# Kernel tuning notes

Measured on AMD Instinct MI355X. Metric: run time of the kernel, lower is better.

Reference implementation:

```python
import jax, jax.numpy as jnp
import numpy as np

V, C, H, W = 6, 256, 128, 128


def setup_inputs() -> dict:
    key = jax.random.key(0)
    ks = jax.random.split(key, 6)
    return {
        "q": jax.random.normal(ks[0], (V, C, H, W), dtype=jnp.float32),
        "k": jax.random.normal(ks[1], (V, C, H, W), dtype=jnp.float32),
        "v": jax.random.normal(ks[2], (V, C, H, W), dtype=jnp.float32),
        "Wq": jax.random.normal(ks[3], (C, C), dtype=jnp.float32) * (1.0 / np.sqrt(C)),
        "Wk": jax.random.normal(ks[4], (C, C), dtype=jnp.float32) * (1.0 / np.sqrt(C)),
        "Wv": jax.random.normal(ks[5], (C, C), dtype=jnp.float32) * (1.0 / np.sqrt(C)),
    }


def reference(q, k, v, Wq, Wk, Wv):
    # 1x1 conv (no bias) == channel GEMM: [V,C,H,W] x [O,C] -> [V,O,H,W]
    qp = jnp.einsum("vchw,oc->vohw", q, Wq)
    kp = jnp.einsum("vchw,oc->vohw", k, Wk)
    vp = jnp.einsum("vchw,oc->vohw", v, Wv)
    # elementwise q*k, sum over channels (dim=1, keepdim) -> [V,1,H,W]
    att = jnp.sum(qp * kp, axis=1, keepdims=True)
    # softmax over views (dim=0)
    att = jax.nn.softmax(att, axis=0)
    # weight values and sum over views (dim=0, keepdim) -> [1,C,H,W]
    out = jnp.sum(att * vp, axis=0, keepdims=True)
    return out
```

## Files before the change

### kernel.cpp

```cpp
#include <hip/hip_runtime.h>
#include <math.h>

#define HW 16384
#define C_DIM 256
#define V_DIM 6
#define PT 64
#define BK 32
#define KROW 40

typedef short bf16x8 __attribute__((ext_vector_type(8)));
typedef float f32x4 __attribute__((ext_vector_type(4)));

__device__ __forceinline__ void split2(float x, unsigned short& h,
                                       unsigned short& l) {
    unsigned u = __float_as_uint(x);
    h = (unsigned short)(u >> 16);
    float xl = x - __uint_as_float(u & 0xFFFF0000u);
    l = (unsigned short)(__float_as_uint(xl) >> 16);
}

__global__ void compute_M_kernel(const float* __restrict__ Wq,
                                 const float* __restrict__ Wk,
                                 unsigned short* __restrict__ Mh,
                                 unsigned short* __restrict__ Ml) {
    const int i = blockIdx.x;
    const int j = threadIdx.x;
    float a0 = 0.f, a1 = 0.f, a2 = 0.f, a3 = 0.f;
    #pragma unroll 4
    for (int o = 0; o < C_DIM; o += 4) {
        a0 = fmaf(Wq[(o + 0) * C_DIM + i], Wk[(o + 0) * C_DIM + j], a0);
        a1 = fmaf(Wq[(o + 1) * C_DIM + i], Wk[(o + 1) * C_DIM + j], a1);
        a2 = fmaf(Wq[(o + 2) * C_DIM + i], Wk[(o + 2) * C_DIM + j], a2);
        a3 = fmaf(Wq[(o + 3) * C_DIM + i], Wk[(o + 3) * C_DIM + j], a3);
    }
    float acc = (a0 + a1) + (a2 + a3);
    unsigned short h, l;
    split2(acc, h, l);
    Mh[i * C_DIM + j] = h;
    Ml[i * C_DIM + j] = l;
}

__global__ __launch_bounds__(512, 4) void score_kernel(
        const float* __restrict__ q, const float* __restrict__ k,
        const unsigned short* __restrict__ Mh,
        const unsigned short* __restrict__ Ml,
        float* __restrict__ score) {
    const int tid  = threadIdx.x;
    const int lane = tid & 63;
    const int w    = tid >> 6;
    const int pt   = blockIdx.x & 255;
    const int v    = blockIdx.x >> 8;
    const int gp0  = pt * PT;
    const int l15  = lane & 15;
    const int l4   = lane >> 4;

    __shared__ __align__(16) unsigned short Kh_s[2][PT * KROW];
    __shared__ __align__(16) unsigned short Kl_s[2][PT * KROW];
    __shared__ float s_red[8][PT];

    const float* kv = k + (size_t)v * C_DIM * HW + gp0;
    const float* qv = q + (size_t)v * C_DIM * HW + gp0;
    const int ibase = w * 32;

    f32x4 acc[2][4];
    #pragma unroll
    for (int a = 0; a < 2; ++a)
        #pragma unroll
        for (int b = 0; b < 4; ++b)
            acc[a][b] = (f32x4){0.f, 0.f, 0.f, 0.f};

    float kx[2][4];
    bf16x8 Ah[2][2], Al[2][2];

    {
        const float* kp = kv + (size_t)(w * 4) * HW + lane;
        float x[4];
        #pragma unroll
        for (int e = 0; e < 4; ++e) x[e] = kp[(size_t)e * HW];
        unsigned short h[4], l[4];
        #pragma unroll
        for (int e = 0; e < 4; ++e) split2(x[e], h[e], l[e]);
        uint2 H, L;
        H.x = (unsigned)h[0] | ((unsigned)h[1] << 16);
        H.y = (unsigned)h[2] | ((unsigned)h[3] << 16);
        L.x = (unsigned)l[0] | ((unsigned)l[1] << 16);
        L.y = (unsigned)l[2] | ((unsigned)l[3] << 16);
        *(uint2*)&Kh_s[0][lane * KROW + w * 4] = H;
        *(uint2*)&Kl_s[0][lane * KROW + w * 4] = L;

        const float* kp1 = kv + (size_t)(BK + w * 4) * HW + lane;
        #pragma unroll
        for (int e = 0; e < 4; ++e) kx[1][e] = kp1[(size_t)e * HW];

        #pragma unroll
        for (int it = 0; it < 2; ++it) {
            int row = ibase + it * 16 + l15;
            Ah[0][it] = *(const bf16x8*)(Mh + (size_t)row * C_DIM + l4 * 8);
            Al[0][it] = *(const bf16x8*)(Ml + (size_t)row * C_DIM + l4 * 8);
        }
    }
    __syncthreads();

    #pragma unroll
    for (int ks = 0; ks < 8; ++ks) {
        const int cur = ks & 1;

        if (ks < 7) {
            #pragma unroll
            for (int it = 0; it < 2; ++it) {
                int row = ibase + it * 16 + l15;
                Ah[cur ^ 1][it] = *(const bf16x8*)(Mh + (size_t)row * C_DIM +
                                                   (ks + 1) * BK + l4 * 8);
                Al[cur ^ 1][it] = *(const bf16x8*)(Ml + (size_t)row * C_DIM +
                                                   (ks + 1) * BK + l4 * 8);
            }
        }
        if (ks < 6) {
            const float* kp = kv + (size_t)((ks + 2) * BK + w * 4) * HW + lane;
            #pragma unroll
            for (int e = 0; e < 4; ++e) kx[cur][e] = kp[(size_t)e * HW];
        }

        bf16x8 Bh[4];
        #pragma unroll
        for (int jt = 0; jt < 4; ++jt) {
            int bp = jt * 16 + l15;
            Bh[jt] = *(const bf16x8*)&Kh_s[cur][bp * KROW + l4 * 8];
        }
        #pragma unroll
        for (int it = 0; it < 2; ++it)
            #pragma unroll
            for (int jt = 0; jt < 4; ++jt)
                acc[it][jt] = __builtin_amdgcn_mfma_f32_16x16x32_bf16(
                                  Ah[cur][it], Bh[jt], acc[it][jt], 0, 0, 0);
        #pragma unroll
        for (int it = 0; it < 2; ++it)
            #pragma unroll
            for (int jt = 0; jt < 4; ++jt)
                acc[it][jt] = __builtin_amdgcn_mfma_f32_16x16x32_bf16(
                                  Al[cur][it], Bh[jt], acc[it][jt], 0, 0, 0);
        bf16x8 Bl[4];
        #pragma unroll
        for (int jt = 0; jt < 4; ++jt) {
            int bp = jt * 16 + l15;
            Bl[jt] = *(const bf16x8*)&Kl_s[cur][bp * KROW + l4 * 8];
        }
        #pragma unroll
        for (int it = 0; it < 2; ++it)
            #pragma unroll
            for (int jt = 0; jt < 4; ++jt)
                acc[it][jt] = __builtin_amdgcn_mfma_f32_16x16x32_bf16(
                                  Ah[cur][it], Bl[jt], acc[it][jt], 0, 0, 0);

        if (ks < 7) {
            unsigned short h[4], l[4];
            #pragma unroll
            for (int e = 0; e < 4; ++e) split2(kx[cur ^ 1][e], h[e], l[e]);
            uint2 H, L;
            H.x = (unsigned)h[0] | ((unsigned)h[1] << 16);
            H.y = (unsigned)h[2] | ((unsigned)h[3] << 16);
            L.x = (unsigned)l[0] | ((unsigned)l[1] << 16);
            L.y = (unsigned)l[2] | ((unsigned)l[3] << 16);
            *(uint2*)&Kh_s[cur ^ 1][lane * KROW + w * 4] = H;
            *(uint2*)&Kl_s[cur ^ 1][lane * KROW + w * 4] = L;
        }
        __syncthreads();
    }

    float sp[4];
    #pragma unroll
    for (int jt = 0; jt < 4; ++jt) sp[jt] = 0.f;
    #pragma unroll
    for (int jt = 0; jt < 4; ++jt) {
        #pragma unroll
        for (int it = 0; it < 2; ++it) {
            int irow = ibase + it * 16 + l4 * 4;
            const float* qp = qv + (size_t)irow * HW + jt * 16 + l15;
            #pragma unroll
            for (int r = 0; r < 4; ++r)
                sp[jt] = fmaf(qp[(size_t)r * HW], acc[it][jt][r], sp[jt]);
        }
        sp[jt] += __shfl_xor(sp[jt], 16, 64);
        sp[jt] += __shfl_xor(sp[jt], 32, 64);
    }
    if (lane < 16) {
        #pragma unroll
        for (int jt = 0; jt < 4; ++jt)
            s_red[w][jt * 16 + lane] = sp[jt];
    }
    __syncthreads();
    if (tid < PT) {
        float s = 0.f;
        #pragma unroll
        for (int ww = 0; ww < 8; ++ww) s += s_red[ww][tid];
        score[v * HW + gp0 + tid] = s;
    }
}

__global__ __launch_bounds__(256) void softmax_w_kernel(float* __restrict__ score) {
    const int p = blockIdx.x * 256 + threadIdx.x;
    float s[V_DIM];
    float mx = -1e30f;
    #pragma unroll
    for (int vv = 0; vv < V_DIM; ++vv) {
        s[vv] = score[vv * HW + p];
        mx = fmaxf(mx, s[vv]);
    }
    float sum = 0.f;
    #pragma unroll
    for (int vv = 0; vv < V_DIM; ++vv) {
        s[vv] = __expf(s[vv] - mx);
        sum += s[vv];
    }
    float inv = 1.0f / sum;
    #pragma unroll
    for (int vv = 0; vv < V_DIM; ++vv)
        score[vv * HW + p] = s[vv] * inv;
}

__global__ void wsplit_kernel(const float* __restrict__ Wv,
                              unsigned short* __restrict__ Wvh,
                              unsigned short* __restrict__ Wvl) {
    const int i = blockIdx.x;
    const int j = threadIdx.x;
    unsigned short h, l;
    split2(Wv[i * C_DIM + j], h, l);
    Wvh[i * C_DIM + j] = h;
    Wvl[i * C_DIM + j] = l;
}

__global__ __launch_bounds__(512, 2) void out_gemm_kernel(
        const float* __restrict__ vin,
        const unsigned short* __restrict__ Wvh,
        const unsigned short* __restrict__ Wvl,
        const float* __restrict__ wsm,
        float* __restrict__ out) {
    const int tid  = threadIdx.x;
    const int lane = tid & 63;
    const int w    = tid >> 6;
    const int gp0  = blockIdx.x * PT;
    const int l15  = lane & 15;
    const int l4   = lane >> 4;
    const int p_s  = tid & 63;
    const int jg   = tid >> 6;

    __shared__ __align__(16) unsigned short Xh_s[2][PT * KROW];
    __shared__ __align__(16) unsigned short Xl_s[2][PT * KROW];

    float wr[V_DIM];
    #pragma unroll
    for (int vv = 0; vv < V_DIM; ++vv) wr[vv] = wsm[vv * HW + gp0 + p_s];

    const float* vbase = vin + gp0 + p_s;
    const int obase = w * 32;

    f32x4 acc[2][4];
    #pragma unroll
    for (int a = 0; a < 2; ++a)
        #pragma unroll
        for (int b = 0; b < 4; ++b)
            acc[a][b] = (f32x4){0.f, 0.f, 0.f, 0.f};

    bf16x8 Ah[2][2], Al[2][2];

    {
        float xv[4][V_DIM];
        #pragma unroll
        for (int vv = 0; vv < V_DIM; ++vv)
            #pragma unroll
            for (int e = 0; e < 4; ++e)
                xv[e][vv] = vbase[(size_t)(vv * C_DIM + jg * 4 + e) * HW];
        unsigned short h[4], l[4];
        #pragma unroll
        for (int e = 0; e < 4; ++e) {
            float s = 0.f;
            #pragma unroll
            for (int vv = 0; vv < V_DIM; ++vv) s = fmaf(wr[vv], xv[e][vv], s);
            split2(s, h[e], l[e]);
        }
        uint2 H, L;
        H.x = (unsigned)h[0] | ((unsigned)h[1] << 16);
        H.y = (unsigned)h[2] | ((unsigned)h[3] << 16);
        L.x = (unsigned)l[0] | ((unsigned)l[1] << 16);
        L.y = (unsigned)l[2] | ((unsigned)l[3] << 16);
        *(uint2*)&Xh_s[0][p_s * KROW + jg * 4] = H;
        *(uint2*)&Xl_s[0][p_s * KROW + jg * 4] = L;

        #pragma unroll
        for (int it = 0; it < 2; ++it) {
            int row = obase + it * 16 + l15;
            Ah[0][it] = *(const bf16x8*)(Wvh + (size_t)row * C_DIM + l4 * 8);
            Al[0][it] = *(const bf16x8*)(Wvl + (size_t)row * C_DIM + l4 * 8);
        }
    }
    __syncthreads();

    #pragma unroll
    for (int ks = 0; ks < 8; ++ks) {
        const int cur = ks & 1;

        float xv[4][V_DIM];
        if (ks < 7) {
            #pragma unroll
            for (int vv = 0; vv < V_DIM; ++vv)
                #pragma unroll
                for (int e = 0; e < 4; ++e)
                    xv[e][vv] = vbase[(size_t)(vv * C_DIM + (ks + 1) * BK +
                                               jg * 4 + e) * HW];
            #pragma unroll
            for (int it = 0; it < 2; ++it) {
                int row = obase + it * 16 + l15;
                Ah[cur ^ 1][it] = *(const bf16x8*)(Wvh + (size_t)row * C_DIM +
                                                   (ks + 1) * BK + l4 * 8);
                Al[cur ^ 1][it] = *(const bf16x8*)(Wvl + (size_t)row * C_DIM +
                                                   (ks + 1) * BK + l4 * 8);
            }
        }

        bf16x8 Bh[4], Bl[4];
        #pragma unroll
        for (int jt = 0; jt < 4; ++jt) {
            int bp = jt * 16 + l15;
            Bh[jt] = *(const bf16x8*)&Xh_s[cur][bp * KROW + l4 * 8];
            Bl[jt] = *(const bf16x8*)&Xl_s[cur][bp * KROW + l4 * 8];
        }

        #pragma unroll
        for (int it = 0; it < 2; ++it)
            #pragma unroll
            for (int jt = 0; jt < 4; ++jt)
                acc[it][jt] = __builtin_amdgcn_mfma_f32_16x16x32_bf16(
                                  Ah[cur][it], Bh[jt], acc[it][jt], 0, 0, 0);
        #pragma unroll
        for (int it = 0; it < 2; ++it)
            #pragma unroll
            for (int jt = 0; jt < 4; ++jt)
                acc[it][jt] = __builtin_amdgcn_mfma_f32_16x16x32_bf16(
                                  Ah[cur][it], Bl[jt], acc[it][jt], 0, 0, 0);
        #pragma unroll
        for (int it = 0; it < 2; ++it)
            #pragma unroll
            for (int jt = 0; jt < 4; ++jt)
                acc[it][jt] = __builtin_amdgcn_mfma_f32_16x16x32_bf16(
                                  Al[cur][it], Bh[jt], acc[it][jt], 0, 0, 0);

        if (ks < 7) {
            unsigned short h[4], l[4];
            #pragma unroll
            for (int e = 0; e < 4; ++e) {
                float s = 0.f;
                #pragma unroll
                for (int vv = 0; vv < V_DIM; ++vv) s = fmaf(wr[vv], xv[e][vv], s);
                split2(s, h[e], l[e]);
            }
            uint2 H, L;
            H.x = (unsigned)h[0] | ((unsigned)h[1] << 16);
            H.y = (unsigned)h[2] | ((unsigned)h[3] << 16);
            L.x = (unsigned)l[0] | ((unsigned)l[1] << 16);
            L.y = (unsigned)l[2] | ((unsigned)l[3] << 16);
            *(uint2*)&Xh_s[cur ^ 1][p_s * KROW + jg * 4] = H;
            *(uint2*)&Xl_s[cur ^ 1][p_s * KROW + jg * 4] = L;
        }
        __syncthreads();
    }

    #pragma unroll
    for (int it = 0; it < 2; ++it)
        #pragma unroll
        for (int jt = 0; jt < 4; ++jt)
            #pragma unroll
            for (int r = 0; r < 4; ++r) {
                int o = obase + it * 16 + l4 * 4 + r;
                out[(size_t)o * HW + gp0 + jt * 16 + l15] = acc[it][jt][r];
            }
}

extern "C" void kernel_launch(void* const* d_in, const int* in_sizes, int n_in,
                              void* d_out, int out_size, void* d_ws, size_t ws_size,
                              hipStream_t stream) {
    const float* q  = (const float*)d_in[0];
    const float* k  = (const float*)d_in[1];
    const float* v  = (const float*)d_in[2];
    const float* Wq = (const float*)d_in[3];
    const float* Wk = (const float*)d_in[4];
    const float* Wv = (const float*)d_in[5];
    float* out = (float*)d_out;

    unsigned short* Mh = (unsigned short*)d_ws;
    unsigned short* Ml = Mh + C_DIM * C_DIM;
    float* score = (float*)(Ml + C_DIM * C_DIM);

    compute_M_kernel<<<C_DIM, C_DIM, 0, stream>>>(Wq, Wk, Mh, Ml);
    score_kernel<<<V_DIM * 256, 512, 0, stream>>>(q, k, Mh, Ml, score);
    softmax_w_kernel<<<HW / 256, 256, 0, stream>>>(score);
    wsplit_kernel<<<C_DIM, C_DIM, 0, stream>>>(Wv, Mh, Ml);
    out_gemm_kernel<<<HW / PT, 512, 0, stream>>>(v, Mh, Ml, score, out);
}
```

Before: 125.3 us.

## Deepen value prefetch, keep global loads in flight across barriers, shrink LDS padding

Replaces __syncthreads with a barrier that waits only on LDS traffic (lgkmcnt), so global loads issued for later k-steps stay outstanding across the barrier. The output GEMM now prefetches view-weighted value inputs two k-steps ahead using a register double buffer, instead of one. The LDS row stride shrinks from 40 to 34 shorts to change the bank mapping. The trade-offs are more register pressure, and possibly misaligned 8- and 16-byte LDS accesses, since 34-short rows are not 16-byte aligned.

```diff
diff --git a/kernel.cpp b/kernel.cpp
--- a/kernel.cpp
+++ b/kernel.cpp
@@ -6,10 +6,18 @@
 #define V_DIM 6
 #define PT 64
 #define BK 32
-#define KROW 40
+#define KROW 34
 
 typedef short bf16x8 __attribute__((ext_vector_type(8)));
 typedef float f32x4 __attribute__((ext_vector_type(4)));
+
+#define SYNC_KEEP_VM()                                          \
+    do {                                                        \
+        asm volatile("s_waitcnt lgkmcnt(0)" ::: "memory");      \
+        __builtin_amdgcn_sched_barrier(0);                      \
+        __builtin_amdgcn_s_barrier();                           \
+        __builtin_amdgcn_sched_barrier(0);                      \
+    } while (0)
 
 __device__ __forceinline__ void split2(float x, unsigned short& h,
                                        unsigned short& l) {
@@ -99,7 +107,7 @@
             Al[0][it] = *(const bf16x8*)(Ml + (size_t)row * C_DIM + l4 * 8);
         }
     }
-    __syncthreads();
+    SYNC_KEEP_VM();
 
     #pragma unroll
     for (int ks = 0; ks < 8; ++ks) {
@@ -164,7 +172,7 @@
             *(uint2*)&Kh_s[cur ^ 1][lane * KROW + w * 4] = H;
             *(uint2*)&Kl_s[cur ^ 1][lane * KROW + w * 4] = L;
         }
-        __syncthreads();
+        SYNC_KEEP_VM();
     }
 
     float sp[4];
@@ -241,17 +249,16 @@
     const int gp0  = blockIdx.x * PT;
     const int l15  = lane & 15;
     const int l4   = lane >> 4;
-    const int p_s  = tid & 63;
-    const int jg   = tid >> 6;
+    const int jg   = w;
 
     __shared__ __align__(16) unsigned short Xh_s[2][PT * KROW];
     __shared__ __align__(16) unsigned short Xl_s[2][PT * KROW];
 
     float wr[V_DIM];
     #pragma unroll
-    for (int vv = 0; vv < V_DIM; ++vv) wr[vv] = wsm[vv * HW + gp0 + p_s];
-
-    const float* vbase = vin + gp0 + p_s;
+    for (int vv = 0; vv < V_DIM; ++vv) wr[vv] = wsm[vv * HW + gp0 + lane];
+
+    const float* vbase = vin + gp0 + lane;
     const int obase = w * 32;
 
     f32x4 acc[2][4];
@@ -261,21 +268,22 @@
         for (int b = 0; b < 4; ++b)
             acc[a][b] = (f32x4){0.f, 0.f, 0.f, 0.f};
 
+    float vx[2][4][V_DIM];
     bf16x8 Ah[2][2], Al[2][2];
 
     {
-        float xv[4][V_DIM];
+        float x0[4][V_DIM];
         #pragma unroll
         for (int vv = 0; vv < V_DIM; ++vv)
             #pragma unroll
             for (int e = 0; e < 4; ++e)
-                xv[e][vv] = vbase[(size_t)(vv * C_DIM + jg * 4 + e) * HW];
+                x0[e][vv] = vbase[(size_t)(vv * C_DIM + jg * 4 + e) * HW];
         unsigned short h[4], l[4];
         #pragma unroll
         for (int e = 0; e < 4; ++e) {
             float s = 0.f;
             #pragma unroll
-            for (int vv = 0; vv < V_DIM; ++vv) s = fmaf(wr[vv], xv[e][vv], s);
+            for (int vv = 0; vv < V_DIM; ++vv) s = fmaf(wr[vv], x0[e][vv], s);
             split2(s, h[e], l[e]);
         }
         uint2 H, L;
@@ -283,8 +291,14 @@
         H.y = (unsigned)h[2] | ((unsigned)h[3] << 16);
         L.x = (unsigned)l[0] | ((unsigned)l[1] << 16);
         L.y = (unsigned)l[2] | ((unsigned)l[3] << 16);
-        *(uint2*)&Xh_s[0][p_s * KROW + jg * 4] = H;
-        *(uint2*)&Xl_s[0][p_s * KROW + jg * 4] = L;
+        *(uint2*)&Xh_s[0][lane * KROW + jg * 4] = H;
+        *(uint2*)&Xl_s[0][lane * KROW + jg * 4] = L;
+
+        #pragma unroll
+        for (int vv = 0; vv < V_DIM; ++vv)
+            #pragma unroll
+            for (int e = 0; e < 4; ++e)
+                vx[1][e][vv] = vbase[(size_t)(vv * C_DIM + BK + jg * 4 + e) * HW];
 
         #pragma unroll
         for (int it = 0; it < 2; ++it) {
@@ -293,20 +307,13 @@
             Al[0][it] = *(const bf16x8*)(Wvl + (size_t)row * C_DIM + l4 * 8);
         }
     }
-    __syncthreads();
+    SYNC_KEEP_VM();
 
     #pragma unroll
     for (int ks = 0; ks < 8; ++ks) {
         const int cur = ks & 1;
 
-        float xv[4][V_DIM];
         if (ks < 7) {
-            #pragma unroll
-            for (int vv = 0; vv < V_DIM; ++vv)
-                #pragma unroll
-                for (int e = 0; e < 4; ++e)
-                    xv[e][vv] = vbase[(size_t)(vv * C_DIM + (ks + 1) * BK +
-                                               jg * 4 + e) * HW];
             #pragma unroll
             for (int it = 0; it < 2; ++it) {
                 int row = obase + it * 16 + l15;
@@ -316,6 +323,14 @@
                                                    (ks + 1) * BK + l4 * 8);
             }
         }
+        if (ks < 6) {
+            #pragma unroll
+            for (int vv = 0; vv < V_DIM; ++vv)
+                #pragma unroll
+                for (int e = 0; e < 4; ++e)
+                    vx[cur][e][vv] = vbase[(size_t)(vv * C_DIM + (ks + 2) * BK +
+                                                    jg * 4 + e) * HW];
+        }
 
         bf16x8 Bh[4], Bl[4];
         #pragma unroll
@@ -324,7 +339,6 @@
             Bh[jt] = *(const bf16x8*)&Xh_s[cur][bp * KROW + l4 * 8];
             Bl[jt] = *(const bf16x8*)&Xl_s[cur][bp * KROW + l4 * 8];
         }
-
         #pragma unroll
         for (int it = 0; it < 2; ++it)
             #pragma unroll
@@ -350,7 +364,8 @@
             for (int e = 0; e < 4; ++e) {
                 float s = 0.f;
                 #pragma unroll
-                for (int vv = 0; vv < V_DIM; ++vv) s = fmaf(wr[vv], xv[e][vv], s);
+                for (int vv = 0; vv < V_DIM; ++vv)
+                    s = fmaf(wr[vv], vx[cur ^ 1][e][vv], s);
                 split2(s, h[e], l[e]);
             }
             uint2 H, L;
@@ -358,10 +373,10 @@
             H.y = (unsigned)h[2] | ((unsigned)h[3] << 16);
             L.x = (unsigned)l[0] | ((unsigned)l[1] << 16);
             L.y = (unsigned)l[2] | ((unsigned)l[3] << 16);
-            *(uint2*)&Xh_s[cur ^ 1][p_s * KROW + jg * 4] = H;
-            *(uint2*)&Xl_s[cur ^ 1][p_s * KROW + jg * 4] = L;
-        }
-        __syncthreads();
+            *(uint2*)&Xh_s[cur ^ 1][lane * KROW + jg * 4] = H;
+            *(uint2*)&Xl_s[cur ^ 1][lane * KROW + jg * 4] = L;
+        }
+        SYNC_KEEP_VM();
     }
 
     #pragma unroll
```

Result: slower. 135.4 us (+8.1%).
